# Performance work log

Measured on AMD Instinct MI355X. Metric: run time of the kernel, lower is better.

## Reference

```python
import math
import jax, jax.numpy as jnp
import numpy as np

B, L, CIN, COUT = 128, 100, 55, 55
D, H, DFF, MODES = 512, 8, 512, 32
E = D // H
KERNELS = (12, 24)
NK = len(KERNELS)


def _pos_emb(length, d):
    pos = np.arange(length)[:, None].astype(np.float32)
    div = np.exp(np.arange(0, d, 2).astype(np.float32) * (-math.log(10000.0) / d))
    pe = np.zeros((length, d), dtype=np.float32)
    pe[:, 0::2] = np.sin(pos * div)
    pe[:, 1::2] = np.cos(pos * div)
    return jnp.asarray(pe)


def _circ_conv3(x, W):
    # Conv1d(kernel=3, padding=1, padding_mode='circular', bias=False); x:(B,L,C) W:(O,C,3)
    n = x.shape[1]
    xp = jnp.concatenate([x[:, -1:], x, x[:, :1]], axis=1)
    return (jnp.einsum('blc,oc->blo', xp[:, 0:n], W[:, :, 0]) +
            jnp.einsum('blc,oc->blo', xp[:, 1:n + 1], W[:, :, 1]) +
            jnp.einsum('blc,oc->blo', xp[:, 2:n + 2], W[:, :, 2]))


def _moving_avg(x, k):
    # replicate-pad then length-preserving mean filter (Autoformer moving_avg)
    front = jnp.repeat(x[:, :1], (k - 1) // 2, axis=1)
    end = jnp.repeat(x[:, -1:], k // 2, axis=1)
    xp = jnp.concatenate([front, x, end], axis=1)
    c = jnp.cumsum(xp, axis=1)
    c = jnp.concatenate([jnp.zeros_like(c[:, :1]), c], axis=1)
    return (c[:, k:] - c[:, :-k]) / float(k)


def _decomp(x, w, b):
    # series_decomp_multi with learned softmax mixing (Linear(1, NK))
    means = jnp.stack([_moving_avg(x, k) for k in KERNELS], axis=-1)  # (B,L,D,NK)
    mix = jax.nn.softmax(x[..., None] * w + b, axis=-1)
    mean = jnp.sum(means * mix, axis=-1)
    return x - mean, mean


def _my_layernorm(x, g, b):
    mu = x.mean(-1, keepdims=True)
    var = ((x - mu) ** 2).mean(-1, keepdims=True)
    xh = (x - mu) / jnp.sqrt(var + 1e-5) * g + b
    return xh - xh.mean(axis=1, keepdims=True)


def _fourier_block(q, Wc):
    # q:(B,L,H,E) -> rfft over L, per-mode complex GEMM with Wc:(H,E,E,MODES), irfft
    x = jnp.transpose(q, (0, 2, 3, 1))  # (B,H,E,L)
    xf = jnp.fft.rfft(x, axis=-1)
    sel = jnp.einsum('bhem,heom->bhom', xf[..., :MODES], Wc)
    nfreq = x.shape[-1] // 2 + 1
    out_ft = jnp.zeros(sel.shape[:-1] + (nfreq,), sel.dtype).at[..., :MODES].set(sel)
    out = jnp.fft.irfft(out_ft, n=x.shape[-1], axis=-1)
    return jnp.transpose(out, (0, 3, 1, 2))  # (B,L,H,E)


def _fourier_cross(q, k, Wc):
    # FourierCrossAttention: frequency-domain q*k attention with tanh activation, values = k
    xq = jnp.transpose(q, (0, 2, 3, 1))
    xk = jnp.transpose(k, (0, 2, 3, 1))
    qf = jnp.fft.rfft(xq, axis=-1)[..., :MODES]
    kf = jnp.fft.rfft(xk, axis=-1)[..., :MODES]
    qk = jnp.tanh(jnp.einsum('bhex,bhey->bhxy', qf, kf))
    qkv = jnp.einsum('bhxy,bhey->bhex', qk, kf)
    w = jnp.einsum('bhex,heox->bhox', qkv, Wc)
    nfreq = xq.shape[-1] // 2 + 1
    out_ft = jnp.zeros(w.shape[:-1] + (nfreq,), w.dtype).at[..., :MODES].set(w)
    out = jnp.fft.irfft(out_ft / float(D * D), n=xq.shape[-1], axis=-1)
    return jnp.transpose(out, (0, 3, 1, 2))


def _heads(x, W, b):
    y = x @ W.T + b
    return y.reshape(y.shape[0], y.shape[1], H, E)


def _gelu(x):
    return jax.nn.gelu(x, approximate=False)


def _forward(x, emb_enc_w, emb_dec_w, enc_proj_w, enc_proj_b, enc_sig_w, enc_sig_b,
             enc_four_wr, enc_four_wi, enc_ffn_w1, enc_ffn_w2, enc_dcmp_w, enc_dcmp_b,
             enc_norm_g, enc_norm_b, dec_proj_w, dec_proj_b, dec_four_wr, dec_four_wi,
             crs_proj_w, crs_proj_b, crs_four_wr, crs_four_wi, dec_ffn_w1, dec_ffn_w2,
             dec_dcmp_w, dec_dcmp_b, dec_trend_w, dec_norm_g, dec_norm_b,
             out_proj_w, out_proj_b):
    b, n, _ = x.shape
    dist = jnp.abs(jnp.arange(n)[:, None] - jnp.arange(n)[None, :]).astype(x.dtype)
    # seasonal-trend init decomposition
    trend_init = jnp.broadcast_to(x.mean(axis=1, keepdims=True), x.shape)
    seasonal_init = x - trend_init
    pe = _pos_emb(n, D)
    enc_four = enc_four_wr + 1j * enc_four_wi
    enc = _circ_conv3(x, emb_enc_w) + pe
    series_l, prior_l, sigma_l = [], [], []
    for i in range(enc_proj_w.shape[0]):  # e_layers (structurally distinct params)
        Wp, bp = enc_proj_w[i], enc_proj_b[i]
        q = _heads(enc, Wp[0], bp[0])
        k = _heads(enc, Wp[1], bp[1])
        v = _heads(enc, Wp[2], bp[2])  # projected but unused by FourierBlock (faithful)
        attn_out = _fourier_block(q, enc_four).reshape(b, n, D) @ Wp[3].T + bp[3]
        # Anomaly-Transformer association: series = softmax(QK^T/sqrt(E)), prior = Gaussian kernel
        scores = jnp.einsum('blhe,bshe->bhls', q, k) / math.sqrt(E)
        series = jax.nn.softmax(scores, axis=-1)
        sig = jnp.transpose(enc @ enc_sig_w[i].T + enc_sig_b[i], (0, 2, 1))  # (B,H,L)
        sig = jnp.power(3.0, jax.nn.sigmoid(5.0 * sig) + 1e-5) - 1.0
        prior = jnp.exp(-dist ** 2 / (2.0 * sig[..., None] ** 2)) / (math.sqrt(2.0 * math.pi) * sig[..., None])
        series_l.append(series); prior_l.append(prior); sigma_l.append(sig)
        h = enc + attn_out
        h, _ = _decomp(h, enc_dcmp_w[i, 0], enc_dcmp_b[i, 0])
        y = _gelu(h @ enc_ffn_w1[i].T) @ enc_ffn_w2[i].T
        enc, _ = _decomp(h + y, enc_dcmp_w[i, 1], enc_dcmp_b[i, 1])
    enc = _my_layernorm(enc, enc_norm_g, enc_norm_b)

    # decoder (d_layers = 1)
    dec = _circ_conv3(seasonal_init, emb_dec_w) + pe
    dec_four = dec_four_wr + 1j * dec_four_wi
    crs_four = crs_four_wr + 1j * crs_four_wi
    q = _heads(dec, dec_proj_w[0], dec_proj_b[0])
    sa = _fourier_block(q, dec_four).reshape(b, n, D) @ dec_proj_w[3].T + dec_proj_b[3]
    h = dec + sa
    h, t1 = _decomp(h, dec_dcmp_w[0], dec_dcmp_b[0])
    qc = _heads(h, crs_proj_w[0], crs_proj_b[0])
    kc = _heads(enc, crs_proj_w[1], crs_proj_b[1])
    ca = _fourier_cross(qc, kc, crs_four).reshape(b, n, D) @ crs_proj_w[3].T + crs_proj_b[3]
    h = h + ca
    h, t2 = _decomp(h, dec_dcmp_w[1], dec_dcmp_b[1])
    y = _gelu(h @ dec_ffn_w1.T) @ dec_ffn_w2.T
    h, t3 = _decomp(h + y, dec_dcmp_w[2], dec_dcmp_b[2])
    residual_trend = _circ_conv3(t1 + t2 + t3, dec_trend_w)  # (B,L,COUT)
    trend = trend_init + residual_trend
    h = _my_layernorm(h, dec_norm_g, dec_norm_b)
    seasonal = h @ out_proj_w.T + out_proj_b
    dec_out = trend + seasonal
    return dec_out, jnp.stack(series_l), jnp.stack(prior_l), jnp.stack(sigma_l)


def setup_inputs() -> dict:
    key = jax.random.key(0)
    ks = iter(jax.random.split(key, 64))

    def rn(shape, s=0.02):
        return s * jax.random.normal(next(ks), shape, dtype=jnp.float32)

    return dict(
        x=jax.random.normal(next(ks), (B, L, CIN), dtype=jnp.float32),
        emb_enc_w=rn((D, CIN, 3)), emb_dec_w=rn((D, CIN, 3)),
        enc_proj_w=rn((2, 4, D, D)), enc_proj_b=jnp.zeros((2, 4, D), jnp.float32),
        enc_sig_w=rn((2, H, D)), enc_sig_b=jnp.zeros((2, H), jnp.float32),
        enc_four_wr=rn((H, E, E, MODES)), enc_four_wi=rn((H, E, E, MODES)),
        enc_ffn_w1=rn((2, DFF, D)), enc_ffn_w2=rn((2, D, DFF)),
        enc_dcmp_w=rn((2, 2, NK), 1.0), enc_dcmp_b=jnp.zeros((2, 2, NK), jnp.float32),
        enc_norm_g=jnp.ones((D,), jnp.float32), enc_norm_b=jnp.zeros((D,), jnp.float32),
        dec_proj_w=rn((4, D, D)), dec_proj_b=jnp.zeros((4, D), jnp.float32),
        dec_four_wr=rn((H, E, E, MODES)), dec_four_wi=rn((H, E, E, MODES)),
        crs_proj_w=rn((4, D, D)), crs_proj_b=jnp.zeros((4, D), jnp.float32),
        crs_four_wr=rn((H, E, E, MODES)), crs_four_wi=rn((H, E, E, MODES)),
        dec_ffn_w1=rn((DFF, D)), dec_ffn_w2=rn((D, DFF)),
        dec_dcmp_w=rn((3, NK), 1.0), dec_dcmp_b=jnp.zeros((3, NK), jnp.float32),
        dec_trend_w=rn((COUT, D, 3)),
        dec_norm_g=jnp.ones((D,), jnp.float32), dec_norm_b=jnp.zeros((D,), jnp.float32),
        out_proj_w=rn((COUT, D)), out_proj_b=jnp.zeros((COUT,), jnp.float32),
    )


def reference(x, emb_enc_w, emb_dec_w, enc_proj_w, enc_proj_b, enc_sig_w, enc_sig_b,
              enc_four_wr, enc_four_wi, enc_ffn_w1, enc_ffn_w2, enc_dcmp_w, enc_dcmp_b,
              enc_norm_g, enc_norm_b, dec_proj_w, dec_proj_b, dec_four_wr, dec_four_wi,
              crs_proj_w, crs_proj_b, crs_four_wr, crs_four_wi, dec_ffn_w1, dec_ffn_w2,
              dec_dcmp_w, dec_dcmp_b, dec_trend_w, dec_norm_g, dec_norm_b,
              out_proj_w, out_proj_b):
    return _forward(x, emb_enc_w, emb_dec_w, enc_proj_w, enc_proj_b, enc_sig_w, enc_sig_b,
                    enc_four_wr, enc_four_wi, enc_ffn_w1, enc_ffn_w2, enc_dcmp_w, enc_dcmp_b,
                    enc_norm_g, enc_norm_b, dec_proj_w, dec_proj_b, dec_four_wr, dec_four_wi,
                    crs_proj_w, crs_proj_b, crs_four_wr, crs_four_wi, dec_ffn_w1, dec_ffn_w2,
                    dec_dcmp_w, dec_dcmp_b, dec_trend_w, dec_norm_g, dec_norm_b,
                    out_proj_w, out_proj_b)
```

## Files before the change

kernel.cpp:

```cpp
#include <hip/hip_runtime.h>
#include <hip/hip_bf16.h>
#include <cmath>

constexpr int B = 128, L = 100, CIN = 55, COUT = 55;
constexpr int D = 512, H = 8, DFF = 512, MODES = 32, E = 64;
constexpr int NK = 2;
constexpr int M_ROWS = B * L;
constexpr int KEMB = 192;
constexpr size_t BLD  = (size_t)B * L * D;
constexpr size_t BHEM = (size_t)B * H * E * MODES;
constexpr size_t BHLL = (size_t)B * H * L * L;
constexpr float INV_SQRT_2PI = 0.3989422804014327f;

static inline int cdiv(int a, int b) { return (a + b - 1) / b; }

typedef short shortx8 __attribute__((ext_vector_type(8)));
typedef float f32x4 __attribute__((ext_vector_type(4)));

__device__ inline unsigned short f2bf(float f)
{
    unsigned int u = __float_as_uint(f);
    unsigned int r = (u + 0x7FFFu + ((u >> 16) & 1u)) >> 16;
    return (unsigned short)r;
}
__device__ inline unsigned short f2bf_n(float f)
{
    union { __hip_bfloat16 h; unsigned short u; } cv;
    cv.h = __float2bfloat16(f);
    return cv.u;
}
__device__ inline float bf2f(unsigned short u)
{
    union { unsigned int i; float f; } c;
    c.i = (unsigned int)u << 16;
    return c.f;
}

__global__ void init_consts(float* __restrict__ pe)
{
    int idx = blockIdx.x * 256 + threadIdx.x;
    if (idx < L * D) {
        int l = idx / D, d = idx % D;
        int i2 = d & ~1;
        float div = expf((float)i2 * (-logf(10000.f) / (float)D));
        float ang = (float)l * div;
        pe[idx] = (d & 1) ? cosf(ang) : sinf(ang);
    }
}

__global__ void init_tw(unsigned short* __restrict__ twf, unsigned short* __restrict__ twi)
{
    int idx = blockIdx.x * 256 + threadIdx.x;
    if (idx >= 64 * 128) return;
    {
        int mp = idx / 128, t = idx % 128;
        float v = 0.f;
        if (t < L) {
            if (mp < 32) v = cosf(2.f * 3.14159265358979323846f * (float)mp * (float)t / (float)L);
            else v = -sinf(2.f * 3.14159265358979323846f * (float)(mp - 32) * (float)t / (float)L);
        }
        twf[idx] = f2bf(v);
    }
    {
        int t = idx / 64, mp = idx % 64;
        float v = 0.f;
        if (t < L) {
            if (mp == 0) v = 1.f;
            else if (mp < 32) v = 2.f * cosf(2.f * 3.14159265358979323846f * (float)mp * (float)t / (float)L);
            else if (mp == 32) v = 0.f;
            else v = -2.f * sinf(2.f * 3.14159265358979323846f * (float)(mp - 32) * (float)t / (float)L);
        }
        twi[idx] = f2bf(v);
    }
}

__global__ void xmean_kernel(const float* __restrict__ x, float* __restrict__ xm)
{
    int idx = blockIdx.x * 256 + threadIdx.x;
    if (idx >= B * CIN) return;
    int b = idx / CIN, c = idx % CIN;
    float s = 0.f;
    for (int l = 0; l < L; ++l) s += x[((size_t)b * L + l) * CIN + c];
    xm[idx] = s * (1.f / (float)L);
}

struct PrepArgs {
    const float* src[7];
    unsigned short* dst[7];
    int n4[7];
    const float* emb_enc; const float* emb_dec; const float* trend_w; const float* seas_w;
    unsigned short* d_embenc; unsigned short* d_embdec; unsigned short* d_trd; unsigned short* d_seas;
};
__global__ __launch_bounds__(256) void prep_all(PrepArgs a, int total4, int padTotal)
{
    for (int i = blockIdx.x * 256 + threadIdx.x; i < total4 + padTotal; i += gridDim.x * 256) {
        if (i < total4) {
            int idx = i, s = 0;
            while (idx >= a.n4[s]) { idx -= a.n4[s]; ++s; }
            float4 v = *(const float4*)&a.src[s][(size_t)idx * 4];
            ushort4 h;
            h.x = f2bf(v.x); h.y = f2bf(v.y); h.z = f2bf(v.z); h.w = f2bf(v.w);
            *(ushort4*)&a.dst[s][(size_t)idx * 4] = h;
            continue;
        }
        int p = i - total4;
        if (p < D * KEMB) {
            int r = p / KEMB, k = p % KEMB;
            a.d_embenc[p] = (k < CIN * 3) ? f2bf(a.emb_enc[(size_t)r * (CIN * 3) + k]) : (unsigned short)0;
        } else if ((p -= D * KEMB) < D * KEMB) {
            int r = p / KEMB, k = p % KEMB;
            a.d_embdec[p] = (k < CIN * 3) ? f2bf(a.emb_dec[(size_t)r * (CIN * 3) + k]) : (unsigned short)0;
        } else if ((p -= D * KEMB) < 192 * D) {
            int n = p / D, d = p % D;
            int j = n / 64, o = n % 64;
            a.d_trd[p] = (o < COUT) ? f2bf(a.trend_w[(size_t)o * (D * 3) + d * 3 + j]) : (unsigned short)0;
        } else {
            p -= 192 * D;
            int r = p / D, k = p % D;
            a.d_seas[p] = (r < COUT) ? f2bf(a.seas_w[(size_t)r * D + k]) : (unsigned short)0;
        }
    }
}

__global__ __launch_bounds__(256) void transpose_w(const float* __restrict__ wr, const float* __restrict__ wi,
                                                   float2* __restrict__ wt)
{
    int h = blockIdx.x / E, e = blockIdx.x % E;
    __shared__ float tr[64][33], ti[64][33];
    for (int i = threadIdx.x; i < E * MODES; i += 256) {
        int o = i / MODES, m = i % MODES;
        size_t s = (((size_t)h * E + e) * E + o) * MODES + m;
        tr[o][m] = wr[s]; ti[o][m] = wi[s];
    }
    __syncthreads();
    for (int i = threadIdx.x; i < MODES * E; i += 256) {
        int m = i / E, o = i % E;
        wt[(((size_t)h * MODES + m) * E + e) * E + o] = make_float2(tr[o][m], ti[o][m]);
    }
}

__global__ void im2col_emb(const float* __restrict__ x, const float* __restrict__ xmean,
                           unsigned short* __restrict__ A2)
{
    int idx = blockIdx.x * 256 + threadIdx.x;
    if (idx >= M_ROWS * KEMB) return;
    int k = idx % KEMB, m = idx / KEMB;
    float v = 0.f;
    if (k < CIN * 3) {
        int c = k / 3, j = k % 3;
        int l = m % L, b = m / L;
        int ls = l + j - 1; ls = (ls + L) % L;
        v = x[((size_t)b * L + ls) * CIN + c];
        if (xmean) v -= xmean[(size_t)b * CIN + c];
    }
    A2[idx] = f2bf(v);
}

template<int BN>
__global__ __launch_bounds__(256) void gemm_mfma(const unsigned short* __restrict__ A,
                                                 const unsigned short* __restrict__ Wb,
                                                 const float* __restrict__ bias, const float* __restrict__ pe,
                                                 float* __restrict__ C, unsigned short* __restrict__ Cb,
                                                 int Nout, int K, int act, int accum)
{
    constexpr int NI = BN / 32;
    constexpr int BI = BN / 64;
    __shared__ unsigned short As[2][128][40];
    __shared__ unsigned short Bs[2][BN][40];
    int tid = threadIdx.x;
    int row0 = blockIdx.y * 128, col0 = blockIdx.x * BN;
    int wid = tid >> 6, lane = tid & 63;
    int wm = wid >> 1, wn = wid & 1;
    int lrow = lane & 15, kg = lane >> 4;
    int ar = tid >> 2, ac8 = (tid & 3) * 8;
    f32x4 acc[4][NI] = {};
    shortx8 rah[2], rbh[BI];

// ... 40 lines not shown
        if (s + 1 < nk) __syncthreads();
        cur ^= 1;
    }
#pragma unroll
    for (int mi = 0; mi < 4; ++mi) {
#pragma unroll
        for (int ni = 0; ni < NI; ++ni) {
            int col = col0 + wn * (BN / 2) + ni * 16 + lrow;
            if (col >= Nout) continue;
#pragma unroll
            for (int r = 0; r < 4; ++r) {
                int row = row0 + wm * 64 + mi * 16 + kg * 4 + r;
                float v = acc[mi][ni][r];
                if (bias) v += bias[col];
                if (pe) v += pe[(size_t)(row % L) * Nout + col];
                if (act) v = 0.5f * v * (1.f + erff(v * 0.70710678118654752f));
                size_t o = (size_t)row * Nout + col;
                if (Cb) Cb[o] = f2bf_n(v);
                else if (accum) C[o] += v;
                else C[o] = v;
            }
        }
    }
}

__global__ __launch_bounds__(256) void scores_softmax(const unsigned short* __restrict__ QK,
                                                      float* __restrict__ out)
{
    int bh = blockIdx.x, b = bh / H, h = bh % H;
    int pass = blockIdx.y;
    __shared__ unsigned short Ks[112][72];
    __shared__ unsigned short Qs[64][72];
    int tid = threadIdx.x;
    int srow = tid >> 4, sc4 = (tid & 15) * 4;
#pragma unroll
    for (int i = 0; i < 7; ++i) {
        int r = i * 16 + srow;
        ushort4 hh = {0, 0, 0, 0};
        if (r < L) hh = *(const ushort4*)&QK[((size_t)b * L + r) * 1024 + 512 + h * E + sc4];
        *(ushort4*)&Ks[r][sc4] = hh;
    }
#pragma unroll
    for (int i = 0; i < 4; ++i) {
        int r = i * 16 + srow;
        int gr = pass * 64 + r;
        ushort4 hh = {0, 0, 0, 0};
        if (gr < L) hh = *(const ushort4*)&QK[((size_t)b * L + gr) * 1024 + h * E + sc4];
        *(ushort4*)&Qs[r][sc4] = hh;
    }
    __syncthreads();
    int wid = tid >> 6, lane = tid & 63;
    int lrow = lane & 15, kg = lane >> 4;
    f32x4 acc[7] = {};
#pragma unroll
    for (int ks = 0; ks < 2; ++ks) {
        shortx8 aq = *(const shortx8*)&Qs[wid * 16 + lrow][ks * 32 + kg * 8];
#pragma unroll
        for (int tj = 0; tj < 7; ++tj) {
            shortx8 bk = *(const shortx8*)&Ks[tj * 16 + lrow][ks * 32 + kg * 8];
            acc[tj] = __builtin_amdgcn_mfma_f32_16x16x32_bf16(aq, bk, acc[tj], 0, 0, 0);
        }
    }
    float mx[4] = {-1e30f, -1e30f, -1e30f, -1e30f};
#pragma unroll
    for (int tj = 0; tj < 7; ++tj) {
        bool valid = (tj * 16 + lrow) < L;
#pragma unroll
        for (int r = 0; r < 4; ++r) {
            float v = acc[tj][r] * 0.125f;
            acc[tj][r] = valid ? v : -1e30f;
            if (valid) mx[r] = fmaxf(mx[r], v);
        }
    }
#pragma unroll
    for (int off = 1; off < 16; off <<= 1)
#pragma unroll
        for (int r = 0; r < 4; ++r) mx[r] = fmaxf(mx[r], __shfl_xor(mx[r], off));
    float sum[4] = {0.f, 0.f, 0.f, 0.f};
#pragma unroll
    for (int tj = 0; tj < 7; ++tj)
#pragma unroll
        for (int r = 0; r < 4; ++r) {
            float e = expf(acc[tj][r] - mx[r]);
            acc[tj][r] = e;
            sum[r] += e;
        }
#pragma unroll
    for (int off = 1; off < 16; off <<= 1)
#pragma unroll
        for (int r = 0; r < 4; ++r) sum[r] += __shfl_xor(sum[r], off);
    float inv[4];
#pragma unroll
    for (int r = 0; r < 4; ++r) inv[r] = 1.f / sum[r];
    float* base = out + (size_t)bh * L * L;
#pragma unroll
    for (int r = 0; r < 4; ++r) {
        int row = pass * 64 + wid * 16 + kg * 4 + r;
        if (row >= L) continue;
#pragma unroll
        for (int tj = 0; tj < 7; ++tj) {
            int col = tj * 16 + lrow;
            if (col < L) base[(size_t)row * L + col] = acc[tj][r] * inv[r];
        }
    }
}

__global__ void trend_combine(const float* __restrict__ Y, const float* __restrict__ xmean,
                              float* __restrict__ dec_out)
{
    int idx = blockIdx.x * 256 + threadIdx.x;
    if (idx >= B * L * COUT) return;
    int o = idx % COUT; int l = (idx / COUT) % L; int b = idx / (COUT * L);
    int lm = (l + L - 1) % L, lp = (l + 1) % L;
    float v = xmean[(size_t)b * CIN + o]
            + Y[((size_t)b * L + lm) * 192 + o]
            + Y[((size_t)b * L + l ) * 192 + 64 + o]
            + Y[((size_t)b * L + lp) * 192 + 128 + o];
    dec_out[idx] = v;
}

__global__ __launch_bounds__(256) void dft_mfma(const unsigned short* __restrict__ X,
                                                const unsigned short* __restrict__ twf,
                                                float2* __restrict__ xf, int stride)
{
    int b = blockIdx.x / H, h = blockIdx.x % H;
    __shared__ unsigned short Xs[64][136];
    int tid = threadIdx.x;
    for (int i = tid; i < L * E / 4; i += 256) {
        int t = i >> 4, e4 = (i & 15) * 4;
        ushort4 u = *(const ushort4*)&X[((size_t)b * L + t) * stride + h * E + e4];
        Xs[e4][t] = u.x; Xs[e4 + 1][t] = u.y; Xs[e4 + 2][t] = u.z; Xs[e4 + 3][t] = u.w;
    }
    for (int i = tid; i < 64 * 28; i += 256) {
// ... 126 lines not shown
    for (int i = threadIdx.x; i < MODES * E; i += 256) {
        int x = i / E, e = i % E;
        float re = 0.f, im = 0.f;
        for (int y = 0; y < MODES; ++y) {
            float ar = tr[x][y], ai = ti[x][y];
            float2 kk = km[y][e];
            re += ar * kk.x - ai * kk.y;
            im += ar * kk.y + ai * kk.x;
        }
        vm[x][e] = make_float2(re, im);
    }
    __syncthreads();
    for (int i = threadIdx.x; i < MODES * E; i += 256) {
        int m = i / E, e = i % E;
        kf[((size_t)(h * MODES + m) * B + b) * E + e] = vm[m][e];
    }
}

__global__ __launch_bounds__(256) void sigma_prior(const unsigned short* __restrict__ enc,
                                                   const float* __restrict__ w,
                                                   const float* __restrict__ bias,
                                                   float* __restrict__ sig_out, float* __restrict__ prior)
{
    __shared__ float wsh[H][D];
    for (int i = threadIdx.x; i < H * D; i += 256) wsh[i / D][i % D] = w[i];
    __syncthreads();
    int wid = threadIdx.x / 64, lane = threadIdx.x % 64;
    int row = blockIdx.x * 4 + wid;
    const unsigned short* p = enc + (size_t)row * D;
    float xv[8];
#pragma unroll
    for (int i = 0; i < 8; ++i) xv[i] = bf2f(p[lane + i * 64]);
    int b = row / L, l = row % L;
#pragma unroll
    for (int h = 0; h < H; ++h) {
        float s = 0.f;
#pragma unroll
        for (int i = 0; i < 8; ++i) s += xv[i] * wsh[h][lane + i * 64];
        for (int off = 32; off; off >>= 1) s += __shfl_xor(s, off);
        float acc = s + bias[h];
        float sg = 1.f / (1.f + expf(-5.f * acc));
        float val = expf((sg + 1e-5f) * 1.0986122886681098f) - 1.f;
        if (lane == 0) sig_out[((size_t)b * H + h) * L + l] = val;
        float inv2 = 1.f / (2.f * val * val);
        float coef = INV_SQRT_2PI / val;
        float* pr = prior + (((size_t)b * H + h) * L + l) * L;
        for (int sc = lane; sc < L; sc += 64) {
            float d = (float)abs(l - sc);
            pr[sc] = expf(-d * d * inv2) * coef;
        }
    }
}

__global__ __launch_bounds__(256) void decomp_kernel(const unsigned short* __restrict__ in1,
                                                     const unsigned short* __restrict__ in2,
                                                     const float* __restrict__ w, const float* __restrict__ bc,
                                                     unsigned short* __restrict__ res, float* __restrict__ trend,
                                                     unsigned short* __restrict__ trend16, int tmode)
{
    int b = blockIdx.x / (D / 64);
    int d0 = (blockIdx.x % (D / 64)) * 64;
    __shared__ float P[125][65];
    __shared__ float qtot[4][64];
    int tid = threadIdx.x;
    int dd = tid & 63, q = tid >> 6;
// ... 125 lines not shown
    const float* dec_trend_w = (const float*)d_in[27];
    const float* dec_norm_g  = (const float*)d_in[28];
    const float* dec_norm_b  = (const float*)d_in[29];
    const float* out_proj_w  = (const float*)d_in[30];
    const float* out_proj_b  = (const float*)d_in[31];

    float* ws = (float*)d_ws;
    size_t off = 0;
    float* pe    = ws + off; off += (size_t)L * D;
    float* xmean = ws + off; off += (size_t)B * CIN;
    float* bufF  = ws + off; off += BLD;
    float* tacc  = ws + off; off += BLD;
    float2* xfc  = (float2*)(ws + off); off += 2 * BHEM;
    float2* kfc  = (float2*)(ws + off); off += 2 * BHEM;
    float2* wtb  = (float2*)(ws + off); off += 2 * (size_t)H * MODES * E * E;
    unsigned short* qk16 = (unsigned short*)(ws + off); off += BLD;
    unsigned short* e16  = (unsigned short*)(ws + off); off += BLD / 2;
    unsigned short* c16  = (unsigned short*)(ws + off); off += BLD / 2;
    unsigned short* d16  = (unsigned short*)(ws + off); off += BLD / 2;
    unsigned short* h16  = (unsigned short*)(ws + off); off += BLD / 2;
    unsigned short* t16  = (unsigned short*)(ws + off); off += BLD / 2;
    unsigned short* im16 = (unsigned short*)(ws + off); off += (size_t)M_ROWS * KEMB / 2;
    unsigned short* wbf_encproj = (unsigned short*)(ws + off); off += (size_t)2 * 4 * D * D / 2;
    unsigned short* wbf_ffn1    = (unsigned short*)(ws + off); off += (size_t)2 * DFF * D / 2;
    unsigned short* wbf_ffn2    = (unsigned short*)(ws + off); off += (size_t)2 * D * DFF / 2;
    unsigned short* wbf_decproj = (unsigned short*)(ws + off); off += (size_t)4 * D * D / 2;
    unsigned short* wbf_crsproj = (unsigned short*)(ws + off); off += (size_t)4 * D * D / 2;
    unsigned short* wbf_dffn1   = (unsigned short*)(ws + off); off += (size_t)DFF * D / 2;
    unsigned short* wbf_dffn2   = (unsigned short*)(ws + off); off += (size_t)D * DFF / 2;
    unsigned short* wbf_embenc  = (unsigned short*)(ws + off); off += (size_t)D * KEMB / 2;
    unsigned short* wbf_embdec  = (unsigned short*)(ws + off); off += (size_t)D * KEMB / 2;
    unsigned short* wbf_trd     = (unsigned short*)(ws + off); off += (size_t)192 * D / 2;
    unsigned short* wbf_seas    = (unsigned short*)(ws + off); off += (size_t)64 * D / 2;
    unsigned short* twf         = (unsigned short*)(ws + off); off += (size_t)64 * 128 / 2;
    unsigned short* twi         = (unsigned short*)(ws + off); off += (size_t)128 * 64 / 2;
    unsigned short* a16 = qk16;
    unsigned short* b16 = qk16 + BLD;

    float* out       = (float*)d_out;
    float* dec_out   = out;
    float* series_out= out + (size_t)B * L * COUT;
    float* prior_out = series_out + 2 * BHLL;
    float* sigma_out = prior_out + 2 * BHLL;

    const int BH = B * H;

    init_consts<<<200, 256, 0, stream>>>(pe);
    init_tw<<<32, 256, 0, stream>>>(twf, twi);
    xmean_kernel<<<cdiv(B * CIN, 256), 256, 0, stream>>>(x, xmean);

    PrepArgs pa;
    pa.src[0] = enc_proj_w; pa.dst[0] = wbf_encproj; pa.n4[0] = 2 * 4 * D * D / 4;
    pa.src[1] = enc_ffn_w1; pa.dst[1] = wbf_ffn1;    pa.n4[1] = 2 * DFF * D / 4;
    pa.src[2] = enc_ffn_w2; pa.dst[2] = wbf_ffn2;    pa.n4[2] = 2 * D * DFF / 4;
    pa.src[3] = dec_proj_w; pa.dst[3] = wbf_decproj; pa.n4[3] = 4 * D * D / 4;
    pa.src[4] = crs_proj_w; pa.dst[4] = wbf_crsproj; pa.n4[4] = 4 * D * D / 4;
    pa.src[5] = dec_ffn_w1; pa.dst[5] = wbf_dffn1;   pa.n4[5] = DFF * D / 4;
    pa.src[6] = dec_ffn_w2; pa.dst[6] = wbf_dffn2;   pa.n4[6] = D * DFF / 4;
    pa.emb_enc = emb_enc_w; pa.emb_dec = emb_dec_w; pa.trend_w = dec_trend_w; pa.seas_w = out_proj_w;
    pa.d_embenc = wbf_embenc; pa.d_embdec = wbf_embdec; pa.d_trd = wbf_trd; pa.d_seas = wbf_seas;
    int total4 = 0;
    for (int s = 0; s < 7; ++s) total4 += pa.n4[s];
    int padTotal = 2 * D * KEMB + 192 * D + 64 * D;
    prep_all<<<2048, 256, 0, stream>>>(pa, total4, padTotal);
    transpose_w<<<H * E, 256, 0, stream>>>(enc_four_wr, enc_four_wi, wtb);

    auto gemm = [&](const unsigned short* A, const unsigned short* Wb, const float* bias, const float* pe_,
                    float* C, unsigned short* Cb, int N, int Nout, int K, int act, int accum) {
        if (N % 128 == 0) {
            dim3 grid(N / 128, M_ROWS / 128);
            gemm_mfma<128><<<grid, 256, 0, stream>>>(A, Wb, bias, pe_, C, Cb, Nout, K, act, accum);
        } else {
            dim3 grid(N / 64, M_ROWS / 128);
            gemm_mfma<64><<<grid, 256, 0, stream>>>(A, Wb, bias, pe_, C, Cb, Nout, K, act, accum);
        }
    };
    dim3 mg_grid(H * MODES, B / 32);
    dim3 sc_grid(BH, 2);

    im2col_emb<<<cdiv(M_ROWS * KEMB, 256), 256, 0, stream>>>(x, nullptr, im16);
    gemm(im16, wbf_embenc, nullptr, pe, nullptr, e16, D, D, KEMB, 0, 0);

    for (int i = 0; i < 2; ++i) {
        const unsigned short* Wp = wbf_encproj + (size_t)i * 4 * D * D;
        const float* bp = enc_proj_b + (size_t)i * 4 * D;
        float* series_i = series_out + (size_t)i * BHLL;
        float* prior_i  = prior_out  + (size_t)i * BHLL;
        float* sigma_i  = sigma_out  + (size_t)i * B * H * L;

        gemm(e16, Wp, bp, nullptr, nullptr, qk16, 1024, 1024, D, 0, 0);
        dft_mfma<<<BH, 256, 0, stream>>>(qk16, twf, xfc, 1024);
        mode_gemm2<<<mg_grid, 256, 0, stream>>>(xfc, wtb);
        idft_mfma<<<BH, 256, 0, stream>>>(xfc, twi, c16, 1.f / (float)L);
        gemm(c16, Wp + (size_t)3 * D * D, bp + 3 * D, nullptr, nullptr, d16, D, D, D, 0, 0);
        scores_softmax<<<sc_grid, 256, 0, stream>>>(qk16, series_i);
        sigma_prior<<<M_ROWS / 4, 256, 0, stream>>>(e16, enc_sig_w + (size_t)i * H * D,
                                                    enc_sig_b + (size_t)i * H, sigma_i, prior_i);
        decomp_kernel<<<B * (D / 64), 256, 0, stream>>>(e16, d16, enc_dcmp_w + (size_t)(i * 2 + 0) * NK,
                                                        enc_dcmp_b + (size_t)(i * 2 + 0) * NK, h16, nullptr, nullptr, 0);
        gemm(h16, wbf_ffn1 + (size_t)i * DFF * D, nullptr, nullptr, nullptr, c16, DFF, DFF, D, 1, 0);
        gemm(c16, wbf_ffn2 + (size_t)i * D * DFF, nullptr, nullptr, nullptr, d16, D, D, DFF, 0, 0);
        decomp_kernel<<<B * (D / 64), 256, 0, stream>>>(h16, d16, enc_dcmp_w + (size_t)(i * 2 + 1) * NK,
                                                        enc_dcmp_b + (size_t)(i * 2 + 1) * NK, e16, nullptr, nullptr, 0);
    }
    ln_colsub<<<B, 256, 0, stream>>>(e16, enc_norm_g, enc_norm_b, e16);

    transpose_w<<<H * E, 256, 0, stream>>>(dec_four_wr, dec_four_wi, wtb);
    im2col_emb<<<cdiv(M_ROWS * KEMB, 256), 256, 0, stream>>>(x, xmean, im16);
    gemm(im16, wbf_embdec, nullptr, pe, nullptr, a16, D, D, KEMB, 0, 0);
    gemm(a16, wbf_decproj, dec_proj_b, nullptr, nullptr, b16, D, D, D, 0, 0);
    dft_mfma<<<BH, 256, 0, stream>>>(b16, twf, xfc, D);
    mode_gemm2<<<mg_grid, 256, 0, stream>>>(xfc, wtb);
    idft_mfma<<<BH, 256, 0, stream>>>(xfc, twi, c16, 1.f / (float)L);
    gemm(c16, wbf_decproj + (size_t)3 * D * D, dec_proj_b + 3 * D, nullptr, nullptr, d16, D, D, D, 0, 0);
    decomp_kernel<<<B * (D / 64), 256, 0, stream>>>(a16, d16, dec_dcmp_w, dec_dcmp_b, h16, tacc, nullptr, 1);

    gemm(h16, wbf_crsproj, crs_proj_b, nullptr, nullptr, b16, D, D, D, 0, 0);
    dft_mfma<<<BH, 256, 0, stream>>>(b16, twf, xfc, D);
    gemm(e16, wbf_crsproj + (size_t)D * D, crs_proj_b + D, nullptr, nullptr, b16, D, D, D, 0, 0);
    dft_mfma<<<BH, 256, 0, stream>>>(b16, twf, kfc, D);
    transpose_w<<<H * E, 256, 0, stream>>>(crs_four_wr, crs_four_wi, wtb);
    fourier_qk<<<BH, 256, 0, stream>>>(xfc, kfc);
    mode_gemm2<<<mg_grid, 256, 0, stream>>>(kfc, wtb);
    idft_mfma<<<BH, 256, 0, stream>>>(kfc, twi, c16, 1.f / ((float)L * (float)D * (float)D));
    gemm(c16, wbf_crsproj + (size_t)3 * D * D, crs_proj_b + 3 * D, nullptr, nullptr, d16, D, D, D, 0, 0);
    decomp_kernel<<<B * (D / 64), 256, 0, stream>>>(h16, d16, dec_dcmp_w + NK, dec_dcmp_b + NK, a16, tacc, nullptr, 2);

    gemm(a16, wbf_dffn1, nullptr, nullptr, nullptr, c16, DFF, DFF, D, 1, 0);
    gemm(c16, wbf_dffn2, nullptr, nullptr, nullptr, d16, D, D, DFF, 0, 0);
    decomp_kernel<<<B * (D / 64), 256, 0, stream>>>(a16, d16, dec_dcmp_w + 2 * NK, dec_dcmp_b + 2 * NK, b16, tacc, t16, 2);

    gemm(t16, wbf_trd, nullptr, nullptr, bufF, nullptr, 192, 192, D, 0, 0);
    trend_combine<<<cdiv(B * L * COUT, 256), 256, 0, stream>>>(bufF, xmean, dec_out);

    ln_colsub<<<B, 256, 0, stream>>>(b16, dec_norm_g, dec_norm_b, d16);
    gemm(d16, wbf_seas, out_proj_b, nullptr, dec_out, nullptr, 64, COUT, D, 0, 1);
}
```

Baseline: 1.284 ms.

## Merge small setup and epilogue kernels to cut launch count

Several small kernels are folded together. The positional-encoding, twiddle and x-mean setup now runs inside prep_all. The encoder and decoder Fourier weight transposes and the two im2col passes each run as a single launch. scores_softmax and sigma_prior share one grid, split by block index. trend_combine is fused into the final seasonal GEMM epilogue, which now writes dec_out directly instead of accumulating into it. The aim is to remove launch overhead and tail gaps from tiny kernels, at the cost of more branching in the kernels and an extra workspace buffer for the second transposed weight.

Result: no change. 1.307 ms (+1.8%).

```diff
diff --git a/kernel.cpp b/kernel.cpp
--- a/kernel.cpp
+++ b/kernel.cpp
@@ -36,64 +36,20 @@
     return c.f;
 }
 
-__global__ void init_consts(float* __restrict__ pe)
-{
-    int idx = blockIdx.x * 256 + threadIdx.x;
-    if (idx < L * D) {
-        int l = idx / D, d = idx % D;
-        int i2 = d & ~1;
-        float div = expf((float)i2 * (-logf(10000.f) / (float)D));
-        float ang = (float)l * div;
-        pe[idx] = (d & 1) ? cosf(ang) : sinf(ang);
-    }
-}
-
-__global__ void init_tw(unsigned short* __restrict__ twf, unsigned short* __restrict__ twi)
-{
-    int idx = blockIdx.x * 256 + threadIdx.x;
-    if (idx >= 64 * 128) return;
-    {
-        int mp = idx / 128, t = idx % 128;
-        float v = 0.f;
-        if (t < L) {
-            if (mp < 32) v = cosf(2.f * 3.14159265358979323846f * (float)mp * (float)t / (float)L);
-            else v = -sinf(2.f * 3.14159265358979323846f * (float)(mp - 32) * (float)t / (float)L);
-        }
-        twf[idx] = f2bf(v);
-    }
-    {
-        int t = idx / 64, mp = idx % 64;
-        float v = 0.f;
-        if (t < L) {
-            if (mp == 0) v = 1.f;
-            else if (mp < 32) v = 2.f * cosf(2.f * 3.14159265358979323846f * (float)mp * (float)t / (float)L);
-            else if (mp == 32) v = 0.f;
-            else v = -2.f * sinf(2.f * 3.14159265358979323846f * (float)(mp - 32) * (float)t / (float)L);
-        }
-        twi[idx] = f2bf(v);
-    }
-}
-
-__global__ void xmean_kernel(const float* __restrict__ x, float* __restrict__ xm)
-{
-    int idx = blockIdx.x * 256 + threadIdx.x;
-    if (idx >= B * CIN) return;
-    int b = idx / CIN, c = idx % CIN;
-    float s = 0.f;
-    for (int l = 0; l < L; ++l) s += x[((size_t)b * L + l) * CIN + c];
-    xm[idx] = s * (1.f / (float)L);
-}
-
 struct PrepArgs {
     const float* src[7];
     unsigned short* dst[7];
     int n4[7];
     const float* emb_enc; const float* emb_dec; const float* trend_w; const float* seas_w;
     unsigned short* d_embenc; unsigned short* d_embdec; unsigned short* d_trd; unsigned short* d_seas;
+    float* pe; unsigned short* twf; unsigned short* twi;
+    const float* x; float* xmean;
 };
-__global__ __launch_bounds__(256) void prep_all(PrepArgs a, int total4, int padTotal)
-{
-    for (int i = blockIdx.x * 256 + threadIdx.x; i < total4 + padTotal; i += gridDim.x * 256) {
+__global__ __launch_bounds__(256) void prep_all(PrepArgs a, int total4)
+{
+    const int padTotal = 2 * D * KEMB + 192 * D + 64 * D;
+    const int grand = total4 + padTotal + L * D + 64 * 128 + B * CIN;
+    for (int i = blockIdx.x * 256 + threadIdx.x; i < grand; i += gridDim.x * 256) {
         if (i < total4) {
             int idx = i, s = 0;
             while (idx >= a.n4[s]) { idx -= a.n4[s]; ++s; }
@@ -114,11 +70,67 @@
             int n = p / D, d = p % D;
             int j = n / 64, o = n % 64;
             a.d_trd[p] = (o < COUT) ? f2bf(a.trend_w[(size_t)o * (D * 3) + d * 3 + j]) : (unsigned short)0;
-        } else {
-            p -= 192 * D;
+        } else if ((p -= 192 * D) < 64 * D) {
             int r = p / D, k = p % D;
             a.d_seas[p] = (r < COUT) ? f2bf(a.seas_w[(size_t)r * D + k]) : (unsigned short)0;
-        }
+        } else if ((p -= 64 * D) < L * D) {
+            int l = p / D, d = p % D;
+            int i2 = d & ~1;
+            float div = expf((float)i2 * (-logf(10000.f) / (float)D));
+            float ang = (float)l * div;
+            a.pe[p] = (d & 1) ? cosf(ang) : sinf(ang);
+        } else if ((p -= L * D) < 64 * 128) {
+            {
+                int mp = p / 128, t = p % 128;
+                float v = 0.f;
+                if (t < L) {
+                    if (mp < 32) v = cosf(2.f * 3.14159265358979323846f * (float)mp * (float)t / (float)L);
+                    else v = -sinf(2.f * 3.14159265358979323846f * (float)(mp - 32) * (float)t / (float)L);
+                }
+                a.twf[p] = f2bf(v);
+            }
+            {
+                int t = p / 64, mp = p % 64;
+                float v = 0.f;
+                if (t < L) {
+                    if (mp == 0) v = 1.f;
+                    else if (mp < 32) v = 2.f * cosf(2.f * 3.14159265358979323846f * (float)mp * (float)t / (float)L);
+                    else if (mp == 32) v = 0.f;
+                    else v = -2.f * sinf(2.f * 3.14159265358979323846f * (float)(mp - 32) * (float)t / (float)L);
+                }
+                a.twi[p] = f2bf(v);
+            }
+        } else {
+            p -= 64 * 128;
+            int b = p / CIN, c = p % CIN;
+            float s = 0.f;
+            for (int l = 0; l < L; ++l) s += a.x[((size_t)b * L + l) * CIN + c];
+            a.xmean[p] = s * (1.f / (float)L);
+        }
+    }
+}
+
+__global__ __launch_bounds__(256) void transpose_w2(const float* __restrict__ wr0, const float* __restrict__ wi0,
+                                                    float2* __restrict__ wt0,
+                                                    const float* __restrict__ wr1, const float* __restrict__ wi1,
+                                                    float2* __restrict__ wt1)
+{
+    int pair = blockIdx.x / (H * E);
+    int he = blockIdx.x % (H * E);
+    const float* wr = pair ? wr1 : wr0;
+    const float* wi = pair ? wi1 : wi0;
+    float2* wt = pair ? wt1 : wt0;
+    int h = he / E, e = he % E;
+    __shared__ float tr[64][33], ti[64][33];
+    for (int i = threadIdx.x; i < E * MODES; i += 256) {
+        int o = i / MODES, m = i % MODES;
+        size_t s = (((size_t)h * E + e) * E + o) * MODES + m;
+        tr[o][m] = wr[s]; ti[o][m] = wi[s];
+    }
+    __syncthreads();
+    for (int i = threadIdx.x; i < MODES * E; i += 256) {
+        int m = i / E, o = i % E;
+        wt[(((size_t)h * MODES + m) * E + e) * E + o] = make_float2(tr[o][m], ti[o][m]);
     }
 }
 
@@ -139,21 +151,24 @@
     }
 }
 
-__global__ void im2col_emb(const float* __restrict__ x, const float* __restrict__ xmean,
-                           unsigned short* __restrict__ A2)
+__global__ void im2col_emb2(const float* __restrict__ x, const float* __restrict__ xmean,
+                            unsigned short* __restrict__ A2enc, unsigned short* __restrict__ A2dec)
 {
     int idx = blockIdx.x * 256 + threadIdx.x;
-    if (idx >= M_ROWS * KEMB) return;
-    int k = idx % KEMB, m = idx / KEMB;
+    const int half = M_ROWS * KEMB;
+    if (idx >= 2 * half) return;
+    bool dec = idx >= half;
+    int id = dec ? idx - half : idx;
+    int k = id % KEMB, m = id / KEMB;
     float v = 0.f;
     if (k < CIN * 3) {
         int c = k / 3, j = k % 3;
         int l = m % L, b = m / L;
         int ls = l + j - 1; ls = (ls + L) % L;
         v = x[((size_t)b * L + ls) * CIN + c];
-        if (xmean) v -= xmean[(size_t)b * CIN + c];
-    }
-    A2[idx] = f2bf(v);
+        if (dec) v -= xmean[(size_t)b * CIN + c];
+    }
+    (dec ? A2dec : A2enc)[id] = f2bf(v);
 }
 
 template<int BN>
@@ -161,6 +176,7 @@
                                                  const unsigned short* __restrict__ Wb,
                                                  const float* __restrict__ bias, const float* __restrict__ pe,
                                                  float* __restrict__ C, unsigned short* __restrict__ Cb,
+                                                 const float* __restrict__ trendY, const float* __restrict__ xm,
                                                  int Nout, int K, int act, int accum)
 {
     constexpr int NI = BN / 32;
@@ -231,6 +247,14 @@
                 float v = acc[mi][ni][r];
                 if (bias) v += bias[col];
                 if (pe) v += pe[(size_t)(row % L) * Nout + col];
+                if (trendY) {
+                    int b = row / L, l = row % L;
+                    int lm = (l + L - 1) % L, lp = (l + 1) % L;
+                    v += xm[(size_t)b * CIN + col]
+                       + trendY[((size_t)b * L + lm) * 192 + col]
+                       + trendY[((size_t)b * L + l ) * 192 + 64 + col]
+                       + trendY[((size_t)b * L + lp) * 192 + 128 + col];
+                }
                 if (act) v = 0.5f * v * (1.f + erff(v * 0.70710678118654752f));
                 size_t o = (size_t)row * Nout + col;
                 if (Cb) Cb[o] = f2bf_n(v);
@@ -241,99 +265,120 @@
     }
 }
 
-__global__ __launch_bounds__(256) void scores_softmax(const unsigned short* __restrict__ QK,
-                                                      float* __restrict__ out)
-{
-    int bh = blockIdx.x, b = bh / H, h = bh % H;
-    int pass = blockIdx.y;
-    __shared__ unsigned short Ks[112][72];
-    __shared__ unsigned short Qs[64][72];
+__global__ __launch_bounds__(256) void scores_sigma(const unsigned short* __restrict__ QK,
+                                                    const unsigned short* __restrict__ enc,
+                                                    const float* __restrict__ w, const float* __restrict__ bias,
+                                                    float* __restrict__ series,
+                                                    float* __restrict__ sig_out, float* __restrict__ prior)
+{
+    __shared__ char smem[(112 + 64) * 72 * 2];
+    int bid = blockIdx.x;
     int tid = threadIdx.x;
-    int srow = tid >> 4, sc4 = (tid & 15) * 4;
-#pragma unroll
-    for (int i = 0; i < 7; ++i) {
-        int r = i * 16 + srow;
-        ushort4 hh = {0, 0, 0, 0};
-        if (r < L) hh = *(const ushort4*)&QK[((size_t)b * L + r) * 1024 + 512 + h * E + sc4];
-        *(ushort4*)&Ks[r][sc4] = hh;
-    }
-#pragma unroll
-    for (int i = 0; i < 4; ++i) {
-        int r = i * 16 + srow;
-        int gr = pass * 64 + r;
-        ushort4 hh = {0, 0, 0, 0};
-        if (gr < L) hh = *(const ushort4*)&QK[((size_t)b * L + gr) * 1024 + h * E + sc4];
-        *(ushort4*)&Qs[r][sc4] = hh;
-    }
-    __syncthreads();
     int wid = tid >> 6, lane = tid & 63;
-    int lrow = lane & 15, kg = lane >> 4;
-    f32x4 acc[7] = {};
-#pragma unroll
-    for (int ks = 0; ks < 2; ++ks) {
-        shortx8 aq = *(const shortx8*)&Qs[wid * 16 + lrow][ks * 32 + kg * 8];
+    if (bid < 2 * B * H) {
+        auto Ks = (unsigned short(*)[72])smem;
+        auto Qs = (unsigned short(*)[72])(smem + 112 * 72 * 2);
+        int bh = bid >> 1, pass = bid & 1;
+        int b = bh / H, h = bh % H;
+        int srow = tid >> 4, sc4 = (tid & 15) * 4;
+#pragma unroll
+        for (int i = 0; i < 7; ++i) {
+            int r = i * 16 + srow;
+            ushort4 hh = {0, 0, 0, 0};
+            if (r < L) hh = *(const ushort4*)&QK[((size_t)b * L + r) * 1024 + 512 + h * E + sc4];
+            *(ushort4*)&Ks[r][sc4] = hh;
+        }
+#pragma unroll
+        for (int i = 0; i < 4; ++i) {
+            int r = i * 16 + srow;
+            int gr = pass * 64 + r;
+            ushort4 hh = {0, 0, 0, 0};
+            if (gr < L) hh = *(const ushort4*)&QK[((size_t)b * L + gr) * 1024 + h * E + sc4];
+            *(ushort4*)&Qs[r][sc4] = hh;
+        }
+        __syncthreads();
+        int lrow = lane & 15, kg = lane >> 4;
+        f32x4 acc[7] = {};
+#pragma unroll
+        for (int ks = 0; ks < 2; ++ks) {
+            shortx8 aq = *(const shortx8*)&Qs[wid * 16 + lrow][ks * 32 + kg * 8];
+#pragma unroll
+            for (int tj = 0; tj < 7; ++tj) {
+                shortx8 bk = *(const shortx8*)&Ks[tj * 16 + lrow][ks * 32 + kg * 8];
+                acc[tj] = __builtin_amdgcn_mfma_f32_16x16x32_bf16(aq, bk, acc[tj], 0, 0, 0);
+            }
+        }
+        float mx[4] = {-1e30f, -1e30f, -1e30f, -1e30f};
 #pragma unroll
         for (int tj = 0; tj < 7; ++tj) {
-            shortx8 bk = *(const shortx8*)&Ks[tj * 16 + lrow][ks * 32 + kg * 8];
-            acc[tj] = __builtin_amdgcn_mfma_f32_16x16x32_bf16(aq, bk, acc[tj], 0, 0, 0);
-        }
-    }
-    float mx[4] = {-1e30f, -1e30f, -1e30f, -1e30f};
-#pragma unroll
-    for (int tj = 0; tj < 7; ++tj) {
-        bool valid = (tj * 16 + lrow) < L;
+            bool valid = (tj * 16 + lrow) < L;
+#pragma unroll
+            for (int r = 0; r < 4; ++r) {
+                float v = acc[tj][r] * 0.125f;
+                acc[tj][r] = valid ? v : -1e30f;
+                if (valid) mx[r] = fmaxf(mx[r], v);
+            }
+        }
+#pragma unroll
+        for (int off = 1; off < 16; off <<= 1)
+#pragma unroll
+            for (int r = 0; r < 4; ++r) mx[r] = fmaxf(mx[r], __shfl_xor(mx[r], off));
+        float sum[4] = {0.f, 0.f, 0.f, 0.f};
+#pragma unroll
+        for (int tj = 0; tj < 7; ++tj)
+#pragma unroll
+            for (int r = 0; r < 4; ++r) {
+                float e = expf(acc[tj][r] - mx[r]);
+                acc[tj][r] = e;
+                sum[r] += e;
+            }
+#pragma unroll
+        for (int off = 1; off < 16; off <<= 1)
+#pragma unroll
+            for (int r = 0; r < 4; ++r) sum[r] += __shfl_xor(sum[r], off);
+        float inv[4];
+#pragma unroll
+        for (int r = 0; r < 4; ++r) inv[r] = 1.f / sum[r];
+        float* base = series + (size_t)bh * L * L;
 #pragma unroll
         for (int r = 0; r < 4; ++r) {
-            float v = acc[tj][r] * 0.125f;
-            acc[tj][r] = valid ? v : -1e30f;
-            if (valid) mx[r] = fmaxf(mx[r], v);
-        }
-    }
-#pragma unroll
-    for (int off = 1; off < 16; off <<= 1)
-#pragma unroll
-        for (int r = 0; r < 4; ++r) mx[r] = fmaxf(mx[r], __shfl_xor(mx[r], off));
-    float sum[4] = {0.f, 0.f, 0.f, 0.f};
-#pragma unroll
-    for (int tj = 0; tj < 7; ++tj)
-#pragma unroll
-        for (int r = 0; r < 4; ++r) {
-            float e = expf(acc[tj][r] - mx[r]);
-            acc[tj][r] = e;
-            sum[r] += e;
-        }
-#pragma unroll
-    for (int off = 1; off < 16; off <<= 1)
-#pragma unroll
-        for (int r = 0; r < 4; ++r) sum[r] += __shfl_xor(sum[r], off);
-    float inv[4];
-#pragma unroll
-    for (int r = 0; r < 4; ++r) inv[r] = 1.f / sum[r];
-    float* base = out + (size_t)bh * L * L;
-#pragma unroll
-    for (int r = 0; r < 4; ++r) {
-        int row = pass * 64 + wid * 16 + kg * 4 + r;
-        if (row >= L) continue;
-#pragma unroll
-        for (int tj = 0; tj < 7; ++tj) {
-            int col = tj * 16 + lrow;
-            if (col < L) base[(size_t)row * L + col] = acc[tj][r] * inv[r];
-        }
-    }
-}
-
-__global__ void trend_combine(const float* __restrict__ Y, const float* __restrict__ xmean,
-                              float* __restrict__ dec_out)
-{
-    int idx = blockIdx.x * 256 + threadIdx.x;
-    if (idx >= B * L * COUT) return;
-    int o = idx % COUT; int l = (idx / COUT) % L; int b = idx / (COUT * L);
-    int lm = (l + L - 1) % L, lp = (l + 1) % L;
-    float v = xmean[(size_t)b * CIN + o]
-            + Y[((size_t)b * L + lm) * 192 + o]
-            + Y[((size_t)b * L + l ) * 192 + 64 + o]
-            + Y[((size_t)b * L + lp) * 192 + 128 + o];
-    dec_out[idx] = v;
+            int row = pass * 64 + wid * 16 + kg * 4 + r;
+            if (row >= L) continue;
+#pragma unroll
+            for (int tj = 0; tj < 7; ++tj) {
+                int col = tj * 16 + lrow;
+                if (col < L) base[(size_t)row * L + col] = acc[tj][r] * inv[r];
+            }
+        }
+    } else {
+        auto wsh = (float(*)[D])smem;
+        for (int i = tid; i < H * D; i += 256) wsh[i / D][i % D] = w[i];
+        __syncthreads();
+        int row = (bid - 2 * B * H) * 4 + wid;
+        const unsigned short* p = enc + (size_t)row * D;
+        float xv[8];
+#pragma unroll
+        for (int i = 0; i < 8; ++i) xv[i] = bf2f(p[lane + i * 64]);
+        int b = row / L, l = row % L;
+#pragma unroll
+        for (int h = 0; h < H; ++h) {
+            float s = 0.f;
+#pragma unroll
+            for (int i = 0; i < 8; ++i) s += xv[i] * wsh[h][lane + i * 64];
+            for (int off = 32; off; off >>= 1) s += __shfl_xor(s, off);
+            float acc = s + bias[h];
+            float sg = 1.f / (1.f + expf(-5.f * acc));
+            float val = expf((sg + 1e-5f) * 1.0986122886681098f) - 1.f;
+            if (lane == 0) sig_out[((size_t)b * H + h) * L + l] = val;
+            float inv2 = 1.f / (2.f * val * val);
+            float coef = INV_SQRT_2PI / val;
+            float* pr = prior + (((size_t)b * H + h) * L + l) * L;
+            for (int sc = lane; sc < L; sc += 64) {
+                float d = (float)abs(l - sc);
+                pr[sc] = expf(-d * d * inv2) * coef;
+            }
+        }
+    }
 }
 
 __global__ __launch_bounds__(256) void dft_mfma(const unsigned short* __restrict__ X,
@@ -490,41 +535,6 @@
     for (int i = threadIdx.x; i < MODES * E; i += 256) {
         int m = i / E, e = i % E;
         kf[((size_t)(h * MODES + m) * B + b) * E + e] = vm[m][e];
-    }
-}
-
-__global__ __launch_bounds__(256) void sigma_prior(const unsigned short* __restrict__ enc,
-                                                   const float* __restrict__ w,
-                                                   const float* __restrict__ bias,
-                                                   float* __restrict__ sig_out, float* __restrict__ prior)
-{
-    __shared__ float wsh[H][D];
-    for (int i = threadIdx.x; i < H * D; i += 256) wsh[i / D][i % D] = w[i];
-    __syncthreads();
-    int wid = threadIdx.x / 64, lane = threadIdx.x % 64;
-    int row = blockIdx.x * 4 + wid;
-    const unsigned short* p = enc + (size_t)row * D;
-    float xv[8];
-#pragma unroll
-    for (int i = 0; i < 8; ++i) xv[i] = bf2f(p[lane + i * 64]);
-    int b = row / L, l = row % L;
-#pragma unroll
-    for (int h = 0; h < H; ++h) {
-        float s = 0.f;
-#pragma unroll
-        for (int i = 0; i < 8; ++i) s += xv[i] * wsh[h][lane + i * 64];
-        for (int off = 32; off; off >>= 1) s += __shfl_xor(s, off);
-        float acc = s + bias[h];
-        float sg = 1.f / (1.f + expf(-5.f * acc));
-        float val = expf((sg + 1e-5f) * 1.0986122886681098f) - 1.f;
-        if (lane == 0) sig_out[((size_t)b * H + h) * L + l] = val;
-        float inv2 = 1.f / (2.f * val * val);
-        float coef = INV_SQRT_2PI / val;
-        float* pr = prior + (((size_t)b * H + h) * L + l) * L;
-        for (int sc = lane; sc < L; sc += 64) {
-            float d = (float)abs(l - sc);
-            pr[sc] = expf(-d * d * inv2) * coef;
-        }
     }
 }
 
@@ -680,13 +690,15 @@
     float2* xfc  = (float2*)(ws + off); off += 2 * BHEM;
     float2* kfc  = (float2*)(ws + off); off += 2 * BHEM;
     float2* wtb  = (float2*)(ws + off); off += 2 * (size_t)H * MODES * E * E;
+    float2* wtb2 = (float2*)(ws + off); off += 2 * (size_t)H * MODES * E * E;
     unsigned short* qk16 = (unsigned short*)(ws + off); off += BLD;
     unsigned short* e16  = (unsigned short*)(ws + off); off += BLD / 2;
     unsigned short* c16  = (unsigned short*)(ws + off); off += BLD / 2;
     unsigned short* d16  = (unsigned short*)(ws + off); off += BLD / 2;
     unsigned short* h16  = (unsigned short*)(ws + off); off += BLD / 2;
     unsigned short* t16  = (unsigned short*)(ws + off); off += BLD / 2;
-    unsigned short* im16 = (unsigned short*)(ws + off); off += (size_t)M_ROWS * KEMB / 2;
+    unsigned short* im16a = (unsigned short*)(ws + off); off += (size_t)M_ROWS * KEMB / 2;
+    unsigned short* im16b = (unsigned short*)(ws + off); off += (size_t)M_ROWS * KEMB / 2;
     unsigned short* wbf_encproj = (unsigned short*)(ws + off); off += (size_t)2 * 4 * D * D / 2;
     unsigned short* wbf_ffn1    = (unsigned short*)(ws + off); off += (size_t)2 * DFF * D / 2;
     unsigned short* wbf_ffn2    = (unsigned short*)(ws + off); off += (size_t)2 * D * DFF / 2;
@@ -711,10 +723,6 @@
 
     const int BH = B * H;
 
-    init_consts<<<200, 256, 0, stream>>>(pe);
-    init_tw<<<32, 256, 0, stream>>>(twf, twi);
-    xmean_kernel<<<cdiv(B * CIN, 256), 256, 0, stream>>>(x, xmean);
-
     PrepArgs pa;
     pa.src[0] = enc_proj_w; pa.dst[0] = wbf_encproj; pa.n4[0] = 2 * 4 * D * D / 4;
     pa.src[1] = enc_ffn_w1; pa.dst[1] = wbf_ffn1;    pa.n4[1] = 2 * DFF * D / 4;
@@ -725,27 +733,29 @@
     pa.src[6] = dec_ffn_w2; pa.dst[6] = wbf_dffn2;   pa.n4[6] = D * DFF / 4;
     pa.emb_enc = emb_enc_w; pa.emb_dec = emb_dec_w; pa.trend_w = dec_trend_w; pa.seas_w = out_proj_w;
     pa.d_embenc = wbf_embenc; pa.d_embdec = wbf_embdec; pa.d_trd = wbf_trd; pa.d_seas = wbf_seas;
+    pa.pe = pe; pa.twf = twf; pa.twi = twi; pa.x = x; pa.xmean = xmean;
     int total4 = 0;
     for (int s = 0; s < 7; ++s) total4 += pa.n4[s];
-    int padTotal = 2 * D * KEMB + 192 * D + 64 * D;
-    prep_all<<<2048, 256, 0, stream>>>(pa, total4, padTotal);
-    transpose_w<<<H * E, 256, 0, stream>>>(enc_four_wr, enc_four_wi, wtb);
+    prep_all<<<2048, 256, 0, stream>>>(pa, total4);
+    transpose_w2<<<2 * H * E, 256, 0, stream>>>(enc_four_wr, enc_four_wi, wtb,
+                                                dec_four_wr, dec_four_wi, wtb2);
+    im2col_emb2<<<cdiv(2 * M_ROWS * KEMB, 256), 256, 0, stream>>>(x, xmean, im16a, im16b);
 
     auto gemm = [&](const unsigned short* A, const unsigned short* Wb, const float* bias, const float* pe_,
-                    float* C, unsigned short* Cb, int N, int Nout, int K, int act, int accum) {
+                    float* C, unsigned short* Cb, const float* trendY, const float* xm,
+                    int N, int Nout, int K, int act, int accum) {
         if (N % 128 == 0) {
             dim3 grid(N / 128, M_ROWS / 128);
-            gemm_mfma<128><<<grid, 256, 0, stream>>>(A, Wb, bias, pe_, C, Cb, Nout, K, act, accum);
+            gemm_mfma<128><<<grid, 256, 0, stream>>>(A, Wb, bias, pe_, C, Cb, trendY, xm, Nout, K, act, accum);
         } else {
             dim3 grid(N / 64, M_ROWS / 128);
-            gemm_mfma<64><<<grid, 256, 0, stream>>>(A, Wb, bias, pe_, C, Cb, Nout, K, act, accum);
+            gemm_mfma<64><<<grid, 256, 0, stream>>>(A, Wb, bias, pe_, C, Cb, trendY, xm, Nout, K, act, accum);
         }
     };
     dim3 mg_grid(H * MODES, B / 32);
-    dim3 sc_grid(BH, 2);
-
-    im2col_emb<<<cdiv(M_ROWS * KEMB, 256), 256, 0, stream>>>(x, nullptr, im16);
-    gemm(im16, wbf_embenc, nullptr, pe, nullptr, e16, D, D, KEMB, 0, 0);
+    int ss_grid = 2 * BH + M_ROWS / 4;
+
+    gemm(im16a, wbf_embenc, nullptr, pe, nullptr, e16, nullptr, nullptr, D, D, KEMB, 0, 0);
 
     for (int i = 0; i < 2; ++i) {
         const unsigned short* Wp = wbf_encproj + (size_t)i * 4 * D * D;
@@ -754,51 +764,47 @@
         float* prior_i  = prior_out  + (size_t)i * BHLL;
         float* sigma_i  = sigma_out  + (size_t)i * B * H * L;
 
-        gemm(e16, Wp, bp, nullptr, nullptr, qk16, 1024, 1024, D, 0, 0);
+        gemm(e16, Wp, bp, nullptr, nullptr, qk16, nullptr, nullptr, 1024, 1024, D, 0, 0);
         dft_mfma<<<BH, 256, 0, stream>>>(qk16, twf, xfc, 1024);
         mode_gemm2<<<mg_grid, 256, 0, stream>>>(xfc, wtb);
         idft_mfma<<<BH, 256, 0, stream>>>(xfc, twi, c16, 1.f / (float)L);
-        gemm(c16, Wp + (size_t)3 * D * D, bp + 3 * D, nullptr, nullptr, d16, D, D, D, 0, 0);
-        scores_softmax<<<sc_grid, 256, 0, stream>>>(qk16, series_i);
-        sigma_prior<<<M_ROWS / 4, 256, 0, stream>>>(e16, enc_sig_w + (size_t)i * H * D,
-                                                    enc_sig_b + (size_t)i * H, sigma_i, prior_i);
+        gemm(c16, Wp + (size_t)3 * D * D, bp + 3 * D, nullptr, nullptr, d16, nullptr, nullptr, D, D, D, 0, 0);
+        scores_sigma<<<ss_grid, 256, 0, stream>>>(qk16, e16, enc_sig_w + (size_t)i * H * D,
+                                                  enc_sig_b + (size_t)i * H, series_i, sigma_i, prior_i);
         decomp_kernel<<<B * (D / 64), 256, 0, stream>>>(e16, d16, enc_dcmp_w + (size_t)(i * 2 + 0) * NK,
                                                         enc_dcmp_b + (size_t)(i * 2 + 0) * NK, h16, nullptr, nullptr, 0);
-        gemm(h16, wbf_ffn1 + (size_t)i * DFF * D, nullptr, nullptr, nullptr, c16, DFF, DFF, D, 1, 0);
-        gemm(c16, wbf_ffn2 + (size_t)i * D * DFF, nullptr, nullptr, nullptr, d16, D, D, DFF, 0, 0);
+        gemm(h16, wbf_ffn1 + (size_t)i * DFF * D, nullptr, nullptr, nullptr, c16, nullptr, nullptr, DFF, DFF, D, 1, 0);
+        gemm(c16, wbf_ffn2 + (size_t)i * D * DFF, nullptr, nullptr, nullptr, d16, nullptr, nullptr, D, D, DFF, 0, 0);
         decomp_kernel<<<B * (D / 64), 256, 0, stream>>>(h16, d16, enc_dcmp_w + (size_t)(i * 2 + 1) * NK,
                                                         enc_dcmp_b + (size_t)(i * 2 + 1) * NK, e16, nullptr, nullptr, 0);
     }
     ln_colsub<<<B, 256, 0, stream>>>(e16, enc_norm_g, enc_norm_b, e16);
 
-    transpose_w<<<H * E, 256, 0, stream>>>(dec_four_wr, dec_four_wi, wtb);
-    im2col_emb<<<cdiv(M_ROWS * KEMB, 256), 256, 0, stream>>>(x, xmean, im16);
-    gemm(im16, wbf_embdec, nullptr, pe, nullptr, a16, D, D, KEMB, 0, 0);
-    gemm(a16, wbf_decproj, dec_proj_b, nullptr, nullptr, b16, D, D, D, 0, 0);
+    gemm(im16b, wbf_embdec, nullptr, pe, nullptr, a16, nullptr, nullptr, D, D, KEMB, 0, 0);
+    gemm(a16, wbf_decproj, dec_proj_b, nullptr, nullptr, b16, nullptr, nullptr, D, D, D, 0, 0);
     dft_mfma<<<BH, 256, 0, stream>>>(b16, twf, xfc, D);
-    mode_gemm2<<<mg_grid, 256, 0, stream>>>(xfc, wtb);
+    mode_gemm2<<<mg_grid, 256, 0, stream>>>(xfc, wtb2);
     idft_mfma<<<BH, 256, 0, stream>>>(xfc, twi, c16, 1.f / (float)L);
-    gemm(c16, wbf_decproj + (size_t)3 * D * D, dec_proj_b + 3 * D, nullptr, nullptr, d16, D, D, D, 0, 0);
+    gemm(c16, wbf_decproj + (size_t)3 * D * D, dec_proj_b + 3 * D, nullptr, nullptr, d16, nullptr, nullptr, D, D, D, 0, 0);
     decomp_kernel<<<B * (D / 64), 256, 0, stream>>>(a16, d16, dec_dcmp_w, dec_dcmp_b, h16, tacc, nullptr, 1);
 
-    gemm(h16, wbf_crsproj, crs_proj_b, nullptr, nullptr, b16, D, D, D, 0, 0);
+    gemm(h16, wbf_crsproj, crs_proj_b, nullptr, nullptr, b16, nullptr, nullptr, D, D, D, 0, 0);
     dft_mfma<<<BH, 256, 0, stream>>>(b16, twf, xfc, D);
-    gemm(e16, wbf_crsproj + (size_t)D * D, crs_proj_b + D, nullptr, nullptr, b16, D, D, D, 0, 0);
+    gemm(e16, wbf_crsproj + (size_t)D * D, crs_proj_b + D, nullptr, nullptr, b16, nullptr, nullptr, D, D, D, 0, 0);
     dft_mfma<<<BH, 256, 0, stream>>>(b16, twf, kfc, D);
     transpose_w<<<H * E, 256, 0, stream>>>(crs_four_wr, crs_four_wi, wtb);
     fourier_qk<<<BH, 256, 0, stream>>>(xfc, kfc);
     mode_gemm2<<<mg_grid, 256, 0, stream>>>(kfc, wtb);
     idft_mfma<<<BH, 256, 0, stream>>>(kfc, twi, c16, 1.f / ((float)L * (float)D * (float)D));
-    gemm(c16, wbf_crsproj + (size_t)3 * D * D, crs_proj_b + 3 * D, nullptr, nullptr, d16, D, D, D, 0, 0);
+    gemm(c16, wbf_crsproj + (size_t)3 * D * D, crs_proj_b + 3 * D, nullptr, nullptr, d16, nullptr, nullptr, D, D, D, 0, 0);
     decomp_kernel<<<B * (D / 64), 256, 0, stream>>>(h16, d16, dec_dcmp_w + NK, dec_dcmp_b + NK, a16, tacc, nullptr, 2);
 
-    gemm(a16, wbf_dffn1, nullptr, nullptr, nullptr, c16, DFF, DFF, D, 1, 0);
-    gemm(c16, wbf_dffn2, nullptr, nullptr, nullptr, d16, D, D, DFF, 0, 0);
+    gemm(a16, wbf_dffn1, nullptr, nullptr, nullptr, c16, nullptr, nullptr, DFF, DFF, D, 1, 0);
+    gemm(c16, wbf_dffn2, nullptr, nullptr, nullptr, d16, nullptr, nullptr, D, D, DFF, 0, 0);
     decomp_kernel<<<B * (D / 64), 256, 0, stream>>>(a16, d16, dec_dcmp_w + 2 * NK, dec_dcmp_b + 2 * NK, b16, tacc, t16, 2);
 
-    gemm(t16, wbf_trd, nullptr, nullptr, bufF, nullptr, 192, 192, D, 0, 0);
-    trend_combine<<<cdiv(B * L * COUT, 256), 256, 0, stream>>>(bufF, xmean, dec_out);
+    gemm(t16, wbf_trd, nullptr, nullptr, bufF, nullptr, nullptr, nullptr, 192, 192, D, 0, 0);
 
     ln_colsub<<<B, 256, 0, stream>>>(b16, dec_norm_g, dec_norm_b, d16);
-    gemm(d16, wbf_seas, out_proj_b, nullptr, dec_out, nullptr, 64, COUT, D, 0, 1);
-}
+    gemm(d16, wbf_seas, out_proj_b, nullptr, dec_out, nullptr, bufF, xmean, 64, COUT, D, 0, 0);
+}
```
